# Kernel tuning notes

Measured on AMD Instinct MI355X. Metric: run time of the kernel, lower is better.

## Reference

```python
import jax, jax.numpy as jnp
import numpy as np

B, IN, HID, LAT, EH = 32768, 512, 2048, 128, 512
MID = max(HID // 2, LAT * 2)      # 1024
HALF = max(EH // 2, 4)            # 256
EPS = 1e-5
LN10 = float(np.log(10.0))


def setup_inputs() -> dict:
    key = jax.random.key(0)
    ks = jax.random.split(key, 24)
    r = lambda k, shp, s=0.02: (jax.random.normal(k, shp, dtype=jnp.float32) * s)
    d = {
        "x": jax.random.normal(ks[0], (B, IN), dtype=jnp.float32),
        "group_idx": jax.random.randint(ks[1], (B,), 0, 3),
        # encoder: Linear(IN,HID)+BN+ELU, Linear(HID,MID)+BN+ELU, Linear(MID,LAT)
        "e_w1": r(ks[2], (HID, IN)), "e_b1": jnp.zeros((HID,), jnp.float32),
        "e_g1": jnp.ones((HID,), jnp.float32), "e_be1": jnp.zeros((HID,), jnp.float32),
        "e_w2": r(ks[3], (MID, HID)), "e_b2": jnp.zeros((MID,), jnp.float32),
        "e_g2": jnp.ones((MID,), jnp.float32), "e_be2": jnp.zeros((MID,), jnp.float32),
        "e_w3": r(ks[4], (LAT, MID)), "e_b3": jnp.zeros((LAT,), jnp.float32),
        # shared: Linear(LAT+IN,HID)+BN+ELU, Linear(HID,MID)+BN+ELU
        "s_w1": r(ks[5], (HID, LAT + IN)), "s_b1": jnp.zeros((HID,), jnp.float32),
        "s_g1": jnp.ones((HID,), jnp.float32), "s_be1": jnp.zeros((HID,), jnp.float32),
        "s_w2": r(ks[6], (MID, HID)), "s_b2": jnp.zeros((MID,), jnp.float32),
        "s_g2": jnp.ones((MID,), jnp.float32), "s_be2": jnp.zeros((MID,), jnp.float32),
        # 3 expert heads, stacked on leading axis E=3
        "h_w1": r(ks[7], (3, EH, MID)), "h_b1": jnp.zeros((3, EH), jnp.float32),
        "h_w2": r(ks[8], (3, HALF, EH)), "h_b2": jnp.zeros((3, HALF), jnp.float32),
        "h_w3": r(ks[9], (3, HALF)), "h_b3": jnp.zeros((3,), jnp.float32),
    }
    return d


def _bn(h, g, b):
    # BatchNorm1d in training mode: batch mean, biased batch var
    m = jnp.mean(h, axis=0)
    v = jnp.var(h, axis=0)
    return (h - m) * (g / jnp.sqrt(v + EPS)) + b


def _elu(h):
    return jax.nn.elu(h)


def reference(x, group_idx,
              e_w1, e_b1, e_g1, e_be1, e_w2, e_b2, e_g2, e_be2, e_w3, e_b3,
              s_w1, s_b1, s_g1, s_be1, s_w2, s_b2, s_g2, s_be2,
              h_w1, h_b1, h_w2, h_b2, h_w3, h_b3):
    # encoder
    h = _elu(_bn(x @ e_w1.T + e_b1, e_g1, e_be1))
    h = _elu(_bn(h @ e_w2.T + e_b2, e_g2, e_be2))
    latent = h @ e_w3.T + e_b3                              # [B, LAT]
    # shared trunk
    z = jnp.concatenate([latent, x], axis=-1)               # [B, LAT+IN]
    h = _elu(_bn(z @ s_w1.T + s_b1, s_g1, s_be1))
    hidden = _elu(_bn(h @ s_w2.T + s_b2, s_g2, s_be2))      # [B, MID]
    # expert heads: compute all 3 (tiny vs trunk), then select per-row group
    t1 = _elu(jnp.einsum('bm,ehm->ebh', hidden, h_w1) + h_b1[:, None, :])   # [3,B,EH]
    t2 = _elu(jnp.einsum('ebh,efh->ebf', t1, h_w2) + h_b2[:, None, :])      # [3,B,HALF]
    pred_all = jnp.einsum('ebf,ef->eb', t2, h_w3) + h_b3[:, None]           # [3,B]
    pred_raw = jnp.take_along_axis(pred_all, group_idx[None, :], axis=0)[0] # [B]
    pred_log = -jax.nn.softplus(pred_raw)
    pred_prob = jnp.exp(pred_log * jnp.float32(LN10))       # 10 ** pred_log
    return pred_log, pred_prob
```

## Files before the change

### kernel.cpp

```cpp
#include <hip/hip_runtime.h>
#include <math.h>

#define B_    32768
#define LN10_ 2.302585092994046f
#define MT_H  264
#define NBLK  128

typedef __attribute__((ext_vector_type(8))) short short8;
typedef __attribute__((ext_vector_type(4))) float f32x4;

typedef const __attribute__((address_space(1))) void gvoid_t;
typedef __attribute__((address_space(3))) void svoid_t;

__device__ __forceinline__ void gl16(const void* g, void* l) {
  __builtin_amdgcn_global_load_lds((gvoid_t*)g, (svoid_t*)l, 16, 0, 0);
}

__device__ __forceinline__ float bf2f(unsigned int u) {
  union { unsigned int i; float f; } v; v.i = u << 16; return v.f;
}
__device__ __forceinline__ unsigned short f2bf(float f) {
  union { float f; unsigned int i; } v; v.f = f;
  unsigned int x = v.i;
  unsigned int r = x + 0x7FFFu + ((x >> 16) & 1u);
  return (unsigned short)(r >> 16);
}

__global__ __launch_bounds__(256)
void gemm_bt(const unsigned short* __restrict__ A0, int lda,
             const unsigned short* __restrict__ W0, int ldw,
             unsigned short* __restrict__ C0, int ldc,
             int K, const float* __restrict__ bias0, int elu,
             float* __restrict__ st, int Ntot,
             long eA, long eW, long eC, int eBias,
             const int* __restrict__ texp) {
  __shared__ __align__(16) unsigned short lA[128 * 64];
  __shared__ __align__(16) unsigned short lB[128 * 64];
  const int t = threadIdx.x;
  const int nx = gridDim.x, ny = gridDim.y;
  const int f = blockIdx.y * nx + blockIdx.x;
  const int xcd = f & 7, g = f >> 3;
  const int gdiv = g / nx;
  const int mt = xcd * (ny >> 3) + gdiv;
  const int nt = g - gdiv * nx;
  const int mBase = mt * 128;
  const int nBase = nt * 128;
  int e = texp ? texp[mt] : (int)blockIdx.z;
  if (e < 0) return;
  const unsigned short* A = A0 + (size_t)e * eA;
  const unsigned short* W = W0 + (size_t)e * eW;
  unsigned short* C = C0 + (size_t)e * eC;
  const float* bias = bias0 ? (bias0 + (size_t)e * eBias) : nullptr;
  const unsigned short* Ap = A + (size_t)mBase * lda;
  const unsigned short* Wp = W + (size_t)nBase * ldw;
  const int w = t >> 6, l = t & 63;
  const int wr = (w >> 1) * 64, wc = (w & 1) * 64;
  const int lm = l & 15, lg = l >> 4;

  f32x4 acc[4][4];
#pragma unroll
  for (int i = 0; i < 4; ++i)
#pragma unroll
    for (int j = 0; j < 4; ++j) {
      f32x4 z4 = {0.f, 0.f, 0.f, 0.f};
      acc[i][j] = z4;
    }

  for (int k0 = 0; k0 < K; k0 += 64) {
    __syncthreads();
#pragma unroll
    for (int it = 0; it < 4; ++it) {
      int chunk = it * 256 + t;
      int row = chunk >> 3, sc = chunk & 7;
      int gc = (sc ^ (row & 7)) << 3;
      gl16(Ap + (size_t)row * lda + k0 + gc, &lA[chunk * 8]);
      gl16(Wp + (size_t)row * ldw + k0 + gc, &lB[chunk * 8]);
    }
    __syncthreads();
#pragma unroll
    for (int kk = 0; kk < 64; kk += 32) {
      short8 af[4], bfr[4];
#pragma unroll
      for (int i = 0; i < 4; ++i) {
        int ar = wr + i * 16 + lm;
        int ac = (kk >> 3) + lg;
        af[i] = *(const short8*)&lA[ar * 64 + ((ac ^ (ar & 7)) << 3)];
      }
#pragma unroll
      for (int j = 0; j < 4; ++j) {
        int br = wc + j * 16 + lm;
        int bc = (kk >> 3) + lg;
        bfr[j] = *(const short8*)&lB[br * 64 + ((bc ^ (br & 7)) << 3)];
      }
#pragma unroll
      for (int i = 0; i < 4; ++i)
#pragma unroll
        for (int j = 0; j < 4; ++j)
          acc[i][j] = __builtin_amdgcn_mfma_f32_16x16x32_bf16(af[i], bfr[j], acc[i][j], 0, 0, 0);
    }
  }

#pragma unroll
  for (int j = 0; j < 4; ++j) {
    int n = nBase + wc + j * 16 + lm;
    float bj = bias ? bias[n] : 0.f;
    float s = 0.f, q = 0.f;
#pragma unroll
    for (int i = 0; i < 4; ++i) {
      int m0 = mBase + wr + i * 16 + lg * 4;
#pragma unroll
      for (int r = 0; r < 4; ++r) {
        float v = acc[i][j][r] + bj;
        if (elu) v = v > 0.f ? v : expm1f(v);
        s += v; q += v * v;
        C[(size_t)(m0 + r) * ldc + n] = f2bf(v);
      }
    }
    if (st) {
      s += __shfl_xor(s, 16, 64); s += __shfl_xor(s, 32, 64);
      q += __shfl_xor(q, 16, 64); q += __shfl_xor(q, 32, 64);
      if (lg == 0) { atomicAdd(&st[n], s); atomicAdd(&st[Ntot + n], q); }
    }
  }
}

__global__ void bn_apply(unsigned short* __restrict__ Y, const float* __restrict__ st,
                         const float* __restrict__ gam, const float* __restrict__ bet,
                         int N, float invB) {
  size_t i = (size_t)blockIdx.x * blockDim.x + threadIdx.x;
  size_t base = i * 8;
  int col = (int)(base & (size_t)(N - 1));
  float a8[8], b8[8];
#pragma unroll
  for (int k = 0; k < 8; ++k) {
    int c = col + k;
    float m = st[c] * invB;
    float var = st[N + c] * invB - m * m;
    float av = gam[c] * rsqrtf(var + 1e-5f);
    a8[k] = av;
    b8[k] = bet[c] - m * av;
  }
  uint4 u = *(uint4*)&Y[base];
  unsigned int uu[4] = {u.x, u.y, u.z, u.w};
  unsigned int oo[4];
#pragma unroll
  for (int k = 0; k < 4; ++k) {
    float vlo = bf2f(uu[k] & 0xFFFFu);
    float vhi = bf2f(uu[k] >> 16);
    float flo = a8[2 * k] * vlo + b8[2 * k];
    float fhi = a8[2 * k + 1] * vhi + b8[2 * k + 1];
    flo = flo > 0.f ? flo : expm1f(flo);
    fhi = fhi > 0.f ? fhi : expm1f(fhi);
    oo[k] = (unsigned int)f2bf(flo) | ((unsigned int)f2bf(fhi) << 16);
  }
  uint4 o = {oo[0], oo[1], oo[2], oo[3]};
  *(uint4*)&Y[base] = o;
}

__global__ void cast_all(const float* __restrict__ e1, const float* __restrict__ e2,
                         const float* __restrict__ e3, const float* __restrict__ s1,
                         const float* __restrict__ s2, const float* __restrict__ h1,
                         const float* __restrict__ h2, unsigned short* __restrict__ dst) {
  int i4 = blockIdx.x * 256 + threadIdx.x;
  const float* src;
  int rel;
  if (i4 < 786432) {
    if (i4 < 262144) { src = e1; rel = i4; }
    else             { src = e2; rel = i4 - 262144; }
  } else if (i4 < 1146880) {
    if (i4 < 819200) { src = e3; rel = i4 - 786432; }
    else             { src = s1; rel = i4 - 819200; }
  } else if (i4 < 2064384) {
    if (i4 < 1671168) { src = s2; rel = i4 - 1146880; }
    else              { src = h1; rel = i4 - 1671168; }
  } else { src = h2; rel = i4 - 2064384; }
  float4 v = ((const float4*)src)[rel];
  ushort4 o = {f2bf(v.x), f2bf(v.y), f2bf(v.z), f2bf(v.w)};
  ((ushort4*)dst)[i4] = o;
}

__global__ void cast_x(const float* __restrict__ x, unsigned short* __restrict__ z) {
  int i = blockIdx.x * blockDim.x + threadIdx.x;
  int b = i >> 7;
  int c = (i & 127) << 2;
  float4 v = *(const float4*)&x[(size_t)b * 512 + c];
  ushort4 o = {f2bf(v.x), f2bf(v.y), f2bf(v.z), f2bf(v.w)};
  *(ushort4*)&z[(size_t)b * 640 + 128 + c] = o;
}

__global__ void hist_blocks(const int* __restrict__ gidx, int* __restrict__ bcnt) {
  int blk = blockIdx.x;
  int i = blk * 256 + threadIdx.x;
  int e = gidx[i];
  int l = threadIdx.x & 63, w = threadIdx.x >> 6;
  __shared__ int wc[4][3];
  unsigned long long m0 = __ballot(e == 0);
  unsigned long long m1 = __ballot(e == 1);
  unsigned long long m2 = __ballot(e == 2);
  if (l == 0) { wc[w][0] = __popcll(m0); wc[w][1] = __popcll(m1); wc[w][2] = __popcll(m2); }
  __syncthreads();
  if (threadIdx.x < 3)
    bcnt[blk * 3 + threadIdx.x] = wc[0][threadIdx.x] + wc[1][threadIdx.x] +
                                  wc[2][threadIdx.x] + wc[3][threadIdx.x];
}

__global__ void scan_plan(const int* __restrict__ bcnt, int* __restrict__ boff,
                          int* __restrict__ vend, int* __restrict__ texp) {
  __shared__ int sp[4];
  __shared__ int cnt[3];
  int t = threadIdx.x;
  if (t < 3) {
    int s = 0;
    for (int b = 0; b < NBLK; ++b) s += bcnt[b * 3 + t];
    cnt[t] = s;
  }
  __syncthreads();
  if (t == 0) {
    int p = 0;
    for (int e = 0; e < 3; ++e) {
      sp[e] = p; vend[e] = p + cnt[e];
      p += ((cnt[e] + 127) >> 7) << 7;
    }
    sp[3] = p;
  }
  __syncthreads();
  if (t < 3) {
    int run = sp[t];
    for (int b = 0; b < NBLK; ++b) { boff[b * 3 + t] = run; run += bcnt[b * 3 + t]; }
  }
  if (t < MT_H) {
    int r0 = t << 7, e = -1;
    for (int k = 0; k < 3; ++k)
      if (r0 >= sp[k] && r0 < sp[k + 1]) e = k;
    texp[t] = e;
  }
}

__global__ void scatter2(const int* __restrict__ gidx, const int* __restrict__ boff,
                         int* __restrict__ perm) {
  int blk = blockIdx.x;
  int i = blk * 256 + threadIdx.x;
  int e = gidx[i];
  int l = threadIdx.x & 63, w = threadIdx.x >> 6;
  __shared__ int wc[4][3];
  unsigned long long m0 = __ballot(e == 0);
  unsigned long long m1 = __ballot(e == 1);
  unsigned long long m2 = __ballot(e == 2);
  if (l == 0) { wc[w][0] = __popcll(m0); wc[w][1] = __popcll(m1); wc[w][2] = __popcll(m2); }
  __syncthreads();
  unsigned long long me = (e == 0) ? m0 : ((e == 1) ? m1 : m2);
  int rank = __popcll(me & ((1ull << l) - 1ull));
  int woff = 0;
  for (int ww = 0; ww < w; ++ww) woff += wc[ww][e];
  perm[boff[blk * 3 + e] + woff + rank] = i;
}

__global__ void gather_h(const unsigned short* __restrict__ hid, const int* __restrict__ perm,
                         const int* __restrict__ texp, const int* __restrict__ vend,
                         unsigned short* __restrict__ ht) {
  int idx = blockIdx.x * 256 + threadIdx.x;
  int p = idx >> 7, c8 = (idx & 127) << 3;
  int e = texp[p >> 7];
  uint4 v = {0u, 0u, 0u, 0u};
  if (e >= 0 && p < vend[e]) {
    int src = perm[p];
    v = *(const uint4*)&hid[(size_t)src * 1024 + c8];
  }
  *(uint4*)&ht[(size_t)p * 1024 + c8] = v;
}

__global__ void final_pred(const unsigned short* __restrict__ t2, const int* __restrict__ perm,
                           const int* __restrict__ texp, const int* __restrict__ vend,
                           const float* __restrict__ w3, const float* __restrict__ b3,
                           float* __restrict__ out) {
  int p = blockIdx.x * 4 + (threadIdx.x >> 6);
  int l = threadIdx.x & 63;
  int e = texp[p >> 7];
  if (e < 0 || p >= vend[e]) return;
  ushort4 u = *(const ushort4*)&t2[(size_t)p * 256 + l * 4];
  float4 wv = *(const float4*)&w3[e * 256 + l * 4];
  float sum = bf2f(u.x) * wv.x + bf2f(u.y) * wv.y + bf2f(u.z) * wv.z + bf2f(u.w) * wv.w;
#pragma unroll
  for (int off = 32; off; off >>= 1) sum += __shfl_down(sum, off, 64);
  if (l == 0) {
    int orig = perm[p];
    float xr = sum + b3[e];
    float sp = (xr > 0.f) ? (xr + log1pf(expf(-xr))) : log1pf(expf(xr));
    float pl = -sp;
    out[orig] = pl;
    out[B_ + orig] = expf(pl * LN10_);
  }
}

extern "C" void kernel_launch(void* const* d_in, const int* in_sizes, int n_in,
                              void* d_out, int out_size, void* d_ws, size_t ws_size,
                              hipStream_t stream) {
  const float* x    = (const float*)d_in[0];
  const int*   gidx = (const int*)d_in[1];
  const float* e_w1 = (const float*)d_in[2];
  const float* e_g1 = (const float*)d_in[4];
  const float* e_be1= (const float*)d_in[5];
  const float* e_w2 = (const float*)d_in[6];
  const float* e_g2 = (const float*)d_in[8];
  const float* e_be2= (const float*)d_in[9];
  const float* e_w3 = (const float*)d_in[10];
  const float* e_b3 = (const float*)d_in[11];
  const float* s_w1 = (const float*)d_in[12];
  const float* s_g1 = (const float*)d_in[14];
  const float* s_be1= (const float*)d_in[15];
  const float* s_w2 = (const float*)d_in[16];
  const float* s_g2 = (const float*)d_in[18];
  const float* s_be2= (const float*)d_in[19];
  const float* h_w1 = (const float*)d_in[20];
  const float* h_b1 = (const float*)d_in[21];
  const float* h_w2 = (const float*)d_in[22];
  const float* h_b2 = (const float*)d_in[23];
  const float* h_w3 = (const float*)d_in[24];
  const float* h_b3 = (const float*)d_in[25];
  float* out = (float*)d_out;

  char* ws = (char*)d_ws;
  size_t off = 0;
  auto alloc = [&](size_t bytes) -> char* {
    char* p = ws + off;
    off += (bytes + 255) & ~(size_t)255;
    return p;
  };
  unsigned short* wb_e1 = (unsigned short*)alloc((size_t)2048 * 512 * 2);
  unsigned short* wb_e2 = (unsigned short*)alloc((size_t)1024 * 2048 * 2);
  unsigned short* wb_e3 = (unsigned short*)alloc((size_t)128 * 1024 * 2);
  unsigned short* wb_s1 = (unsigned short*)alloc((size_t)2048 * 640 * 2);
  unsigned short* wb_s2 = (unsigned short*)alloc((size_t)1024 * 2048 * 2);
  unsigned short* wb_h1 = (unsigned short*)alloc((size_t)3 * 512 * 1024 * 2);
  unsigned short* wb_h2 = (unsigned short*)alloc((size_t)3 * 256 * 512 * 2);
  unsigned short* z     = (unsigned short*)alloc((size_t)B_ * 640 * 2);
  unsigned short* bufA  = (unsigned short*)alloc((size_t)B_ * 2048 * 2);
  unsigned short* bufB  = (unsigned short*)alloc((size_t)B_ * 1024 * 2);
  float* st = (float*)alloc(12288 * sizeof(float));
  float* st0 = st;
  float* st1 = st + 4096;
  float* st2 = st + 6144;
  float* st3 = st + 10240;
  int* bcnt = (int*)alloc(NBLK * 3 * sizeof(int));
  int* boff = (int*)alloc(NBLK * 3 * sizeof(int));
  int* vend = (int*)alloc(3 * sizeof(int));
  int* texp = (int*)alloc(MT_H * sizeof(int));
  int* perm = (int*)alloc((size_t)MT_H * 128 * sizeof(int));
  unsigned short* ht  = bufA;
  unsigned short* t1p = bufA + (size_t)MT_H * 128 * 1024;
  unsigned short* t2p = z;

  cast_all<<<8448, 256, 0, stream>>>(e_w1, e_w2, e_w3, s_w1, s_w2, h_w1, h_w2, wb_e1);
  cast_x<<<(B_ * 128) / 256, 256, 0, stream>>>(x, z);
  hipMemsetAsync(st, 0, 12288 * sizeof(float), stream);
  hist_blocks<<<NBLK, 256, 0, stream>>>(gidx, bcnt);
  scan_plan<<<1, 512, 0, stream>>>(bcnt, boff, vend, texp);
  scatter2<<<NBLK, 256, 0, stream>>>(gidx, boff, perm);

  gemm_bt<<<dim3(16, 256), 256, 0, stream>>>(z + 128, 640, wb_e1, 512, bufA, 2048, 512,
                                             nullptr, 0, st0, 2048, 0, 0, 0, 0, nullptr);
  bn_apply<<<B_, 256, 0, stream>>>(bufA, st0, e_g1, e_be1, 2048, 1.0f / B_);
  gemm_bt<<<dim3(8, 256), 256, 0, stream>>>(bufA, 2048, wb_e2, 2048, bufB, 1024, 2048,
                                            nullptr, 0, st1, 1024, 0, 0, 0, 0, nullptr);
  bn_apply<<<B_ / 2, 256, 0, stream>>>(bufB, st1, e_g2, e_be2, 1024, 1.0f / B_);
  gemm_bt<<<dim3(1, 256), 256, 0, stream>>>(bufB, 1024, wb_e3, 1024, z, 640, 1024,
                                            e_b3, 0, nullptr, 0, 0, 0, 0, 0, nullptr);
  gemm_bt<<<dim3(16, 256), 256, 0, stream>>>(z, 640, wb_s1, 640, bufA, 2048, 640,
                                             nullptr, 0, st2, 2048, 0, 0, 0, 0, nullptr);
  bn_apply<<<B_, 256, 0, stream>>>(bufA, st2, s_g1, s_be1, 2048, 1.0f / B_);
  gemm_bt<<<dim3(8, 256), 256, 0, stream>>>(bufA, 2048, wb_s2, 2048, bufB, 1024, 2048,
                                            nullptr, 0, st3, 1024, 0, 0, 0, 0, nullptr);
  bn_apply<<<B_ / 2, 256, 0, stream>>>(bufB, st3, s_g2, s_be2, 1024, 1.0f / B_);

  gather_h<<<(MT_H * 128 * 128) / 256, 256, 0, stream>>>(bufB, perm, texp, vend, ht);

  gemm_bt<<<dim3(4, MT_H), 256, 0, stream>>>(ht, 1024, wb_h1, 1024, t1p, 512, 1024,
                                             h_b1, 1, nullptr, 0,
                                             0, (long)512 * 1024, 0, 512, texp);
  gemm_bt<<<dim3(2, MT_H), 256, 0, stream>>>(t1p, 512, wb_h2, 512, t2p, 256, 512,
                                             h_b2, 1, nullptr, 0,
                                             0, (long)256 * 512, 0, 256, texp);

  final_pred<<<(MT_H * 128) / 4, 256, 0, stream>>>(t2p, perm, texp, vend, h_w3, h_b3, out);
}
```

Measured before the change: 1.150 ms.

## Fuse BatchNorm+ELU into downstream GEMM A-load and expert gather; merge casts

Removes two standalone bn_apply passes over the 1024-wide activations. The second encoder BN+ELU is now applied while loading A tiles in a new GEMM kernel for the latent projection, and the shared trunk's final BN+ELU is folded into the expert-row gather. The x cast is merged into the weight cast kernel to save one launch. In exchange, the fused GEMM loads A through registers instead of async global-to-LDS and recomputes the activation per tile, and the gather recomputes BN coefficients per element.

```diff
diff --git a/kernel.cpp b/kernel.cpp
--- a/kernel.cpp
+++ b/kernel.cpp
@@ -124,6 +124,111 @@
   }
 }
 
+__global__ __launch_bounds__(256)
+void gemm_bn_a(const unsigned short* __restrict__ A0, int lda,
+               const unsigned short* __restrict__ W0, int ldw,
+               unsigned short* __restrict__ C0, int ldc,
+               int K, const float* __restrict__ bias,
+               const float* __restrict__ st, const float* __restrict__ gam,
+               const float* __restrict__ bet, float invB) {
+  __shared__ __align__(16) unsigned short lA[128 * 64];
+  __shared__ __align__(16) unsigned short lB[128 * 64];
+  __shared__ float2 abT[1024];
+  const int t = threadIdx.x;
+  const int nx = gridDim.x, ny = gridDim.y;
+  const int f = blockIdx.y * nx + blockIdx.x;
+  const int xcd = f & 7, g = f >> 3;
+  const int gdiv = g / nx;
+  const int mt = xcd * (ny >> 3) + gdiv;
+  const int nt = g - gdiv * nx;
+  const int mBase = mt * 128;
+  const int nBase = nt * 128;
+  const unsigned short* Ap = A0 + (size_t)mBase * lda;
+  const unsigned short* Wp = W0 + (size_t)nBase * ldw;
+  const int w = t >> 6, l = t & 63;
+  const int wr = (w >> 1) * 64, wc = (w & 1) * 64;
+  const int lm = l & 15, lg = l >> 4;
+
+  for (int c = t; c < K; c += 256) {
+    float m = st[c] * invB;
+    float var = st[K + c] * invB - m * m;
+    float a = gam[c] * rsqrtf(var + 1e-5f);
+    float2 ab; ab.x = a; ab.y = bet[c] - m * a;
+    abT[c] = ab;
+  }
+
+  f32x4 acc[4][4];
+#pragma unroll
+  for (int i = 0; i < 4; ++i)
+#pragma unroll
+    for (int j = 0; j < 4; ++j) {
+      f32x4 z4 = {0.f, 0.f, 0.f, 0.f};
+      acc[i][j] = z4;
+    }
+  __syncthreads();
+
+  for (int k0 = 0; k0 < K; k0 += 64) {
+    __syncthreads();
+#pragma unroll
+    for (int it = 0; it < 4; ++it) {
+      int chunk = it * 256 + t;
+      int row = chunk >> 3, sc = chunk & 7;
+      int gc = (sc ^ (row & 7)) << 3;
+      gl16(Wp + (size_t)row * ldw + k0 + gc, &lB[chunk * 8]);
+      uint4 u = *(const uint4*)&Ap[(size_t)row * lda + k0 + gc];
+      unsigned int uu[4] = {u.x, u.y, u.z, u.w};
+      unsigned int oo[4];
+#pragma unroll
+      for (int k = 0; k < 4; ++k) {
+        int c = k0 + gc + 2 * k;
+        float2 ab0 = abT[c], ab1 = abT[c + 1];
+        float vlo = ab0.x * bf2f(uu[k] & 0xFFFFu) + ab0.y;
+        float vhi = ab1.x * bf2f(uu[k] >> 16) + ab1.y;
+        vlo = vlo > 0.f ? vlo : expm1f(vlo);
+        vhi = vhi > 0.f ? vhi : expm1f(vhi);
+        oo[k] = (unsigned int)f2bf(vlo) | ((unsigned int)f2bf(vhi) << 16);
+      }
+      uint4 o = {oo[0], oo[1], oo[2], oo[3]};
+      *(uint4*)&lA[chunk * 8] = o;
+    }
+    __syncthreads();
+#pragma unroll
+    for (int kk = 0; kk < 64; kk += 32) {
+      short8 af[4], bfr[4];
+#pragma unroll
+      for (int i = 0; i < 4; ++i) {
+        int ar = wr + i * 16 + lm;
+        int ac = (kk >> 3) + lg;
+        af[i] = *(const short8*)&lA[ar * 64 + ((ac ^ (ar & 7)) << 3)];
+      }
+#pragma unroll
+      for (int j = 0; j < 4; ++j) {
+        int br = wc + j * 16 + lm;
+        int bc = (kk >> 3) + lg;
+        bfr[j] = *(const short8*)&lB[br * 64 + ((bc ^ (br & 7)) << 3)];
+      }
+#pragma unroll
+      for (int i = 0; i < 4; ++i)
+#pragma unroll
+        for (int j = 0; j < 4; ++j)
+          acc[i][j] = __builtin_amdgcn_mfma_f32_16x16x32_bf16(af[i], bfr[j], acc[i][j], 0, 0, 0);
+    }
+  }
+
+#pragma unroll
+  for (int j = 0; j < 4; ++j) {
+    int n = nBase + wc + j * 16 + lm;
+    float bj = bias[n];
+#pragma unroll
+    for (int i = 0; i < 4; ++i) {
+      int m0 = mBase + wr + i * 16 + lg * 4;
+#pragma unroll
+      for (int r = 0; r < 4; ++r)
+        C0[(size_t)(m0 + r) * ldc + n] = f2bf(acc[i][j][r] + bj);
+    }
+  }
+}
+
 __global__ void bn_apply(unsigned short* __restrict__ Y, const float* __restrict__ st,
                          const float* __restrict__ gam, const float* __restrict__ bet,
                          int N, float invB) {
@@ -160,8 +265,17 @@
 __global__ void cast_all(const float* __restrict__ e1, const float* __restrict__ e2,
                          const float* __restrict__ e3, const float* __restrict__ s1,
                          const float* __restrict__ s2, const float* __restrict__ h1,
-                         const float* __restrict__ h2, unsigned short* __restrict__ dst) {
+                         const float* __restrict__ h2, const float* __restrict__ x,
+                         unsigned short* __restrict__ wdst, unsigned short* __restrict__ z) {
   int i4 = blockIdx.x * 256 + threadIdx.x;
+  if (i4 >= 2162688) {
+    int rel = i4 - 2162688;
+    int b = rel >> 7, c = (rel & 127) << 2;
+    float4 v = *(const float4*)&x[(size_t)b * 512 + c];
+    ushort4 o = {f2bf(v.x), f2bf(v.y), f2bf(v.z), f2bf(v.w)};
+    *(ushort4*)&z[(size_t)b * 640 + 128 + c] = o;
+    return;
+  }
   const float* src;
   int rel;
   if (i4 < 786432) {
@@ -176,16 +290,7 @@
   } else { src = h2; rel = i4 - 2064384; }
   float4 v = ((const float4*)src)[rel];
   ushort4 o = {f2bf(v.x), f2bf(v.y), f2bf(v.z), f2bf(v.w)};
-  ((ushort4*)dst)[i4] = o;
-}
-
-__global__ void cast_x(const float* __restrict__ x, unsigned short* __restrict__ z) {
-  int i = blockIdx.x * blockDim.x + threadIdx.x;
-  int b = i >> 7;
-  int c = (i & 127) << 2;
-  float4 v = *(const float4*)&x[(size_t)b * 512 + c];
-  ushort4 o = {f2bf(v.x), f2bf(v.y), f2bf(v.z), f2bf(v.w)};
-  *(ushort4*)&z[(size_t)b * 640 + 128 + c] = o;
+  ((ushort4*)wdst)[i4] = o;
 }
 
 __global__ void hist_blocks(const int* __restrict__ gidx, int* __restrict__ bcnt) {
@@ -255,18 +360,37 @@
   perm[boff[blk * 3 + e] + woff + rank] = i;
 }
 
-__global__ void gather_h(const unsigned short* __restrict__ hid, const int* __restrict__ perm,
-                         const int* __restrict__ texp, const int* __restrict__ vend,
-                         unsigned short* __restrict__ ht) {
+__global__ void gather_bn(const unsigned short* __restrict__ hid, const int* __restrict__ perm,
+                          const int* __restrict__ texp, const int* __restrict__ vend,
+                          const float* __restrict__ st, const float* __restrict__ gam,
+                          const float* __restrict__ bet, float invB,
+                          unsigned short* __restrict__ ht) {
   int idx = blockIdx.x * 256 + threadIdx.x;
   int p = idx >> 7, c8 = (idx & 127) << 3;
   int e = texp[p >> 7];
-  uint4 v = {0u, 0u, 0u, 0u};
+  uint4 o = {0u, 0u, 0u, 0u};
   if (e >= 0 && p < vend[e]) {
     int src = perm[p];
-    v = *(const uint4*)&hid[(size_t)src * 1024 + c8];
-  }
-  *(uint4*)&ht[(size_t)p * 1024 + c8] = v;
+    uint4 u = *(const uint4*)&hid[(size_t)src * 1024 + c8];
+    unsigned int uu[4] = {u.x, u.y, u.z, u.w};
+    unsigned int oo[4];
+#pragma unroll
+    for (int k = 0; k < 4; ++k) {
+      int c = c8 + 2 * k;
+      float m0 = st[c] * invB, m1 = st[c + 1] * invB;
+      float v0 = st[1024 + c] * invB - m0 * m0;
+      float v1 = st[1024 + c + 1] * invB - m1 * m1;
+      float a0 = gam[c] * rsqrtf(v0 + 1e-5f);
+      float a1 = gam[c + 1] * rsqrtf(v1 + 1e-5f);
+      float flo = a0 * bf2f(uu[k] & 0xFFFFu) + (bet[c] - m0 * a0);
+      float fhi = a1 * bf2f(uu[k] >> 16) + (bet[c + 1] - m1 * a1);
+      flo = flo > 0.f ? flo : expm1f(flo);
+      fhi = fhi > 0.f ? fhi : expm1f(fhi);
+      oo[k] = (unsigned int)f2bf(flo) | ((unsigned int)f2bf(fhi) << 16);
+    }
+    o.x = oo[0]; o.y = oo[1]; o.z = oo[2]; o.w = oo[3];
+  }
+  *(uint4*)&ht[(size_t)p * 1024 + c8] = o;
 }
 
 __global__ void final_pred(const unsigned short* __restrict__ t2, const int* __restrict__ perm,
@@ -350,8 +474,7 @@
   unsigned short* t1p = bufA + (size_t)MT_H * 128 * 1024;
   unsigned short* t2p = z;
 
-  cast_all<<<8448, 256, 0, stream>>>(e_w1, e_w2, e_w3, s_w1, s_w2, h_w1, h_w2, wb_e1);
-  cast_x<<<(B_ * 128) / 256, 256, 0, stream>>>(x, z);
+  cast_all<<<24832, 256, 0, stream>>>(e_w1, e_w2, e_w3, s_w1, s_w2, h_w1, h_w2, x, wb_e1, z);
   hipMemsetAsync(st, 0, 12288 * sizeof(float), stream);
   hist_blocks<<<NBLK, 256, 0, stream>>>(gidx, bcnt);
   scan_plan<<<1, 512, 0, stream>>>(bcnt, boff, vend, texp);
@@ -362,17 +485,16 @@
   bn_apply<<<B_, 256, 0, stream>>>(bufA, st0, e_g1, e_be1, 2048, 1.0f / B_);
   gemm_bt<<<dim3(8, 256), 256, 0, stream>>>(bufA, 2048, wb_e2, 2048, bufB, 1024, 2048,
                                             nullptr, 0, st1, 1024, 0, 0, 0, 0, nullptr);
-  bn_apply<<<B_ / 2, 256, 0, stream>>>(bufB, st1, e_g2, e_be2, 1024, 1.0f / B_);
-  gemm_bt<<<dim3(1, 256), 256, 0, stream>>>(bufB, 1024, wb_e3, 1024, z, 640, 1024,
-                                            e_b3, 0, nullptr, 0, 0, 0, 0, 0, nullptr);
+  gemm_bn_a<<<dim3(1, 256), 256, 0, stream>>>(bufB, 1024, wb_e3, 1024, z, 640, 1024,
+                                              e_b3, st1, e_g2, e_be2, 1.0f / B_);
   gemm_bt<<<dim3(16, 256), 256, 0, stream>>>(z, 640, wb_s1, 640, bufA, 2048, 640,
                                              nullptr, 0, st2, 2048, 0, 0, 0, 0, nullptr);
   bn_apply<<<B_, 256, 0, stream>>>(bufA, st2, s_g1, s_be1, 2048, 1.0f / B_);
   gemm_bt<<<dim3(8, 256), 256, 0, stream>>>(bufA, 2048, wb_s2, 2048, bufB, 1024, 2048,
                                             nullptr, 0, st3, 1024, 0, 0, 0, 0, nullptr);
-  bn_apply<<<B_ / 2, 256, 0, stream>>>(bufB, st3, s_g2, s_be2, 1024, 1.0f / B_);
-
-  gather_h<<<(MT_H * 128 * 128) / 256, 256, 0, stream>>>(bufB, perm, texp, vend, ht);
+
+  gather_bn<<<(MT_H * 128 * 128) / 256, 256, 0, stream>>>(bufB, perm, texp, vend,
+                                                          st3, s_g2, s_be2, 1.0f / B_, ht);
 
   gemm_bt<<<dim3(4, MT_H), 256, 0, stream>>>(ht, 1024, wb_h1, 1024, t1p, 512, 1024,
                                              h_b1, 1, nullptr, 0,
```

After: 1.160 ms. No clear change (+0.8%).
